# Performance work log

Measured on AMD Instinct MI355X. Metric: run time of the kernel, lower is better.

The kernel has to match this reference:

```python
import jax, jax.numpy as jnp
import numpy as np

NUM_IMU = 72
NUM_NOISE = 12
MAX_PROP = 300
LN_EPS = 1e-5

def _softplus(x):
    return jax.nn.softplus(x)

def setup_inputs() -> dict:
    key = jax.random.key(0)
    k1, k2, k3, k4, k5 = jax.random.split(key, 5)
    d_model = 1024
    seq_len = 4096
    hidden_states = jax.random.normal(k1, (1, seq_len, d_model), dtype=jnp.float32)
    ln_gamma = jnp.ones((d_model,), dtype=jnp.float32)
    ln_beta = jnp.zeros((d_model,), dtype=jnp.float32)
    # Linear: d_model -> NUM_IMU * NUM_NOISE
    W = jax.random.normal(k2, (d_model, NUM_IMU * NUM_NOISE), dtype=jnp.float32) / np.sqrt(d_model)
    b = jax.random.normal(k3, (NUM_IMU * NUM_NOISE,), dtype=jnp.float32) * 0.01
    return {"hidden_states": hidden_states, "ln_gamma": ln_gamma, "ln_beta": ln_beta, "W": W, "b": b}

def _forward(hidden_states, ln_gamma, ln_beta, W, b):
    seq_len = hidden_states.shape[1]
    tsteps = min(MAX_PROP, seq_len)
    x = hidden_states[0]  # [seq, d_model] (squeeze batch=1)
    mu = jnp.mean(x, axis=-1, keepdims=True)
    var = jnp.mean((x - mu) ** 2, axis=-1, keepdims=True)
    xn = (x - mu) * jax.lax.rsqrt(var + LN_EPS) * ln_gamma + ln_beta
    # noise params: [seq, NUM_NOISE, NUM_IMU]
    p = (xn @ W + b).reshape(seq_len, NUM_NOISE, NUM_IMU)
    c = p[:, 4, :]
    c_theta = p[:, 5, :]
    phi = p[:, 6, :]
    phi_theta = p[:, 7, :]
    d = _softplus(p[:, 1, :])
    k = d ** 2 / 4 + _softplus(p[:, 0, :])
    d_theta = _softplus(p[:, 3, :])
    k_theta = d_theta ** 2 / 4 + _softplus(p[:, 2, :])
    acc_base = p[:, 8, :].T      # [imu, seq]
    acc_std = _softplus(p[:, 9, :]).T
    gyro_base = p[:, 10, :].T
    gyro_std = _softplus(p[:, 11, :]).T
    # vectorize over imu: move to [imu, seq, 1]
    def I(a):
        return a.T[:, :, None]
    t = jnp.arange(tsteps, dtype=jnp.float32)[None, None, :]  # [1,1,tstep]
    k_, d_, phi_, c_ = I(k), I(d), I(phi), I(c)
    kt_, dt_, pht_, ct_ = I(k_theta), I(d_theta), I(phi_theta), I(c_theta)
    omega1 = jnp.sqrt(k_ * 4 - d_ ** 2) / 2
    lin = c_ * jnp.exp(-d_ / 2 * t) * jnp.sin(t * omega1 + phi_)
    omega2 = jnp.sqrt(kt_ * 4 - dt_ ** 2) / 2
    ang = ct_ * jnp.exp(-dt_ / 2 * t) * jnp.sin(t * omega2 + pht_)
    spring = lin + ang  # [imu, seq, tstep]
    # banded scatter-add: out[s+t] += spring[:, s, t] for s+t < seq_len
    pos = jnp.arange(seq_len, dtype=jnp.int32)[:, None] + jnp.arange(tsteps, dtype=jnp.int32)[None, :]
    pos_flat = pos.reshape(-1)
    mask = pos_flat < seq_len
    pos_safe = jnp.where(mask, pos_flat, 0)
    vals = spring.reshape(NUM_IMU, -1) * mask.astype(spring.dtype)
    kinematics = jnp.zeros((NUM_IMU, seq_len), dtype=spring.dtype).at[:, pos_safe].add(vals)
    return kinematics, acc_base, acc_std, gyro_base, gyro_std

def reference(hidden_states, ln_gamma, ln_beta, W, b):
    return _forward(hidden_states, ln_gamma, ln_beta, W, b)
```

## Files before the change

### kernel.cpp

```cpp
#include <hip/hip_runtime.h>
#include <hip/hip_bf16.h>
#include <math.h>

#define SEQ 4096
#define DM  1024
#define NIMU 72
#define NNOISE 12
#define NJ (NIMU*NNOISE)
#define TSTEPS 300
#define PLANE (NIMU*SEQ)

#define A2F_SHORTS ((size_t)128 * 128 * 512)
#define BTF_SHORTS ((size_t)28 * 128 * 512)

typedef __attribute__((ext_vector_type(8))) short bf16x8;
typedef __attribute__((ext_vector_type(16))) float f32x16;
typedef __attribute__((ext_vector_type(4))) float f32x4;
typedef __attribute__((ext_vector_type(2))) float f32x2;

__device__ __forceinline__ float softplus_f(float x) {
    return fmaxf(x, 0.f) + log1pf(expf(-fabsf(x)));
}

__device__ __forceinline__ void split_bf16(float x, short& hi, short& lo) {
    unsigned b = __float_as_uint(x);
    unsigned h = (b + 0x7FFFu + ((b >> 16) & 1u)) >> 16;
    float hf = __uint_as_float(h << 16);
    float r = x - hf;
    unsigned b2 = __float_as_uint(r);
    unsigned l2 = (b2 + 0x7FFFu + ((b2 >> 16) & 1u)) >> 16;
    hi = (short)h;
    lo = (short)l2;
}

__global__ __launch_bounds__(512) void ln_kernel(const float* __restrict__ x,
                                                 const float* __restrict__ gamma,
                                                 const float* __restrict__ beta,
                                                 short* __restrict__ A2f) {
    const int tid = threadIdx.x;
    const int row = blockIdx.x * 16 + (tid >> 5);
    const int c   = tid & 31;
    const float4* xr = (const float4*)(x + (size_t)row * DM);

    float s = 0.f, sq = 0.f;
    #pragma unroll
    for (int i = 0; i < 8; ++i) {
        float4 v = xr[c + 32 * i];
        s  += v.x + v.y + v.z + v.w;
        sq += v.x*v.x + v.y*v.y + v.z*v.z + v.w*v.w;
    }
    #pragma unroll
    for (int off = 1; off < 32; off <<= 1) {
        s  += __shfl_xor(s, off);
        sq += __shfl_xor(sq, off);
    }
    const float mean = s * (1.f / DM);
    const float var  = sq * (1.f / DM) - mean * mean;
    const float rstd = rsqrtf(fmaxf(var, 0.f) + 1e-5f);

    const int s_tile = row >> 5, r = row & 31;
    #pragma unroll
    for (int i = 0; i < 8; ++i) {
        const int c4 = c + 32 * i;
        float4 v  = xr[c4];
        float4 gm = ((const float4*)gamma)[c4];
        float4 bt = ((const float4*)beta)[c4];
        float o[4];
        o[0] = (v.x - mean) * rstd * gm.x + bt.x;
        o[1] = (v.y - mean) * rstd * gm.y + bt.y;
        o[2] = (v.z - mean) * rstd * gm.z + bt.z;
        o[3] = (v.w - mean) * rstd * gm.w + bt.w;
        short4 hv, lv;
        split_bf16(o[0], hv.x, lv.x);
        split_bf16(o[1], hv.y, lv.y);
        split_bf16(o[2], hv.z, lv.z);
        split_bf16(o[3], hv.w, lv.w);
        const int ch = c4 >> 2;
        const int g  = (c4 >> 1) & 1;
        const int o4 = (c4 & 1) * 4;
        const size_t base = ((size_t)s_tile * 128 + ch) * 512 + (g * 32 + r) * 8 + o4;
        *(short4*)(A2f + base)                    = hv;
        *(short4*)(A2f + base + (size_t)64 * 512) = lv;
    }
}

__global__ __launch_bounds__(256) void wprep_kernel(const float* __restrict__ W,
                                                    short* __restrict__ Btf) {
    __shared__ float T[32][33];
    const int k0 = blockIdx.x * 32, j0 = blockIdx.y * 32;
    const int t = threadIdx.x;
    {
        const int r = t >> 3, c4 = (t & 7) * 4;
        float4 v = *(const float4*)(W + (size_t)(k0 + r) * NJ + j0 + c4);
        T[r][c4 + 0] = v.x; T[r][c4 + 1] = v.y; T[r][c4 + 2] = v.z; T[r][c4 + 3] = v.w;
    }
    __syncthreads();
    if (t < 128) {
        const int q = t >> 6;
        const int l = t & 63;
        const int n = l & 31, g = l >> 5;
        const int jt = blockIdx.y;
        const int ch = blockIdx.x * 2 + q;
        bf16x8 hv, lv;
        #pragma unroll
        for (int o = 0; o < 8; ++o) {
            short h, lo_;
            split_bf16(T[q * 16 + g * 8 + o][n], h, lo_);
            hv[o] = h; lv[o] = lo_;
        }
        short* dh = Btf + ((size_t)jt * 128 + ch) * 512 + l * 8;
        *(bf16x8*)dh = hv;
        *(bf16x8*)(dh + (size_t)64 * 512) = lv;
    }
}

__global__ __launch_bounds__(256, 2) void gemm_kernel(const short* __restrict__ A2f,
                                                      const short* __restrict__ Btf,
                                                      const float* __restrict__ bias,
                                                      float* __restrict__ ptA,
                                                      float* __restrict__ ptB) {
    const int bid = blockIdx.x;
    const int c = bid & 7, u = bid >> 3;
    const int kh = u / 28, v = u - kh * 28;
    const int bxi = v / 7, by = v - bxi * 7;
    const int bx = c * 4 + bxi;
    const int l = threadIdx.x & 63, w = threadIdx.x >> 6;
    const int mt0 = bx * 4 + (w & 1) * 2;
    const int jt0 = by * 4 + (w >> 1) * 2;
    const int ch0 = kh * 32;
    const short* aB = A2f + (size_t)mt0 * (128 * 512) + l * 8;
    const short* bB = Btf + (size_t)jt0 * (128 * 512) + l * 8;

    f32x16 acc[2][2] = {};
    bf16x8 ah[2][2], al[2][2], bh[2][2], bl[2][2];

    auto ldstep = [&](int slot, int i) {
        const size_t chh = ch0 + i, chl = chh + 64;
        #pragma unroll
        for (int t = 0; t < 2; ++t) {
            ah[slot][t] = *(const bf16x8*)(aB + ((size_t)t * 128 + chh) * 512);
            al[slot][t] = *(const bf16x8*)(aB + ((size_t)t * 128 + chl) * 512);
            bh[slot][t] = *(const bf16x8*)(bB + ((size_t)t * 128 + chh) * 512);
            bl[slot][t] = *(const bf16x8*)(bB + ((size_t)t * 128 + chl) * 512);
        }
    };

    ldstep(0, 0);
    #pragma unroll 2
    for (int i = 0; i < 32; ++i) {
        const int cur = i & 1;
        if (i + 1 < 32) ldstep(cur ^ 1, i + 1);
        #pragma unroll
        for (int mi = 0; mi < 2; ++mi)
            #pragma unroll
            for (int ni = 0; ni < 2; ++ni)
                acc[mi][ni] = __builtin_amdgcn_mfma_f32_32x32x16_bf16(
                    ah[cur][mi], bh[cur][ni], acc[mi][ni], 0, 0, 0);
        #pragma unroll
        for (int mi = 0; mi < 2; ++mi)
            #pragma unroll
            for (int ni = 0; ni < 2; ++ni)
                acc[mi][ni] = __builtin_amdgcn_mfma_f32_32x32x16_bf16(
                    ah[cur][mi], bl[cur][ni], acc[mi][ni], 0, 0, 0);
        #pragma unroll
        for (int mi = 0; mi < 2; ++mi)
            #pragma unroll
            for (int ni = 0; ni < 2; ++ni)
                acc[mi][ni] = __builtin_amdgcn_mfma_f32_32x32x16_bf16(
                    al[cur][mi], bh[cur][ni], acc[mi][ni], 0, 0, 0);
    }

    float* ptH = kh ? ptB : ptA;
    const int jn = l & 31, hi5 = l >> 5;
    #pragma unroll
    for (int ni = 0; ni < 2; ++ni) {
        const int jt = jt0 + ni;
        if (jt < 27) {
            const int j = jt * 32 + jn;
            const float bj = (kh == 0) ? bias[j] : 0.f;
            #pragma unroll
            for (int mi = 0; mi < 2; ++mi) {
                #pragma unroll
                for (int q = 0; q < 4; ++q) {
                    f32x4 o;
                    o[0] = acc[mi][ni][q * 4 + 0] + bj;
                    o[1] = acc[mi][ni][q * 4 + 1] + bj;
                    o[2] = acc[mi][ni][q * 4 + 2] + bj;
                    o[3] = acc[mi][ni][q * 4 + 3] + bj;
                    const int s = (mt0 + mi) * 32 + q * 8 + hi5 * 4;
                    *(f32x4*)(ptH + (size_t)j * SEQ + s) = o;
                }
            }
        }
    }
}

__global__ __launch_bounds__(256) void spring_kernel(const float* __restrict__ ptA,
                                                     const float* __restrict__ ptB,
                                                     float* __restrict__ kin) {
    __shared__ float w3[3][4 * 368];
    const int tid  = threadIdx.x;
    const int lane = tid & 63;
    const int wid  = tid >> 6;
    const int s0   = blockIdx.x * 256;
    const int imu  = blockIdx.y;
    const int s    = s0 + (wid << 6) + lane;

    #pragma unroll
    for (int b = 0; b < 3; ++b)
        #pragma unroll
        for (int i = 0; i < 6; ++i) {
            const int idx = lane + i * 64;
            if (idx < 363) w3[b][wid * 368 + idx] = 0.f;
        }

    const int base = imu * SEQ + s;
    const float p0  = ptA[(size_t)0 * PLANE + base] + ptB[(size_t)0 * PLANE + base];
    const float p1  = ptA[(size_t)1 * PLANE + base] + ptB[(size_t)1 * PLANE + base];
    const float p2  = ptA[(size_t)2 * PLANE + base] + ptB[(size_t)2 * PLANE + base];
    const float p3  = ptA[(size_t)3 * PLANE + base] + ptB[(size_t)3 * PLANE + base];
    const float c1  = ptA[(size_t)4 * PLANE + base] + ptB[(size_t)4 * PLANE + base];
    const float c2  = ptA[(size_t)5 * PLANE + base] + ptB[(size_t)5 * PLANE + base];
    const float ph1 = ptA[(size_t)6 * PLANE + base] + ptB[(size_t)6 * PLANE + base];
    const float ph2 = ptA[(size_t)7 * PLANE + base] + ptB[(size_t)7 * PLANE + base];

    float dd = softplus_f(p1);
    float kk = dd * dd * 0.25f + softplus_f(p0);
    float om1 = 0.5f * sqrtf(fmaxf(4.f * kk - dd * dd, 0.f));
    float dt = softplus_f(p3);
    float kt = dt * dt * 0.25f + softplus_f(p2);
    float om2 = 0.5f * sqrtf(fmaxf(4.f * kt - dt * dt, 0.f));
    float e1 = expf(-0.5f * dd), e2 = expf(-0.5f * dt);
    float sn, cs, sn2, cs2;
    sincosf(om1, &sn, &cs);
    sincosf(om2, &sn2, &cs2);
    f32x2 Rr = {e1 * cs, e2 * cs2};
    f32x2 Ri = {e1 * sn, e2 * sn2};
    sincosf(ph1, &sn, &cs);
    sincosf(ph2, &sn2, &cs2);
    f32x2 zr = {c1 * cs, c2 * cs2};
    f32x2 zi = {c1 * sn, c2 * sn2};

    f32x2 zrB, ziB;
    {
        f32x2 prr = Rr, pri = Ri;
        f32x2 qr = {1.f, 1.f}, qi = {0.f, 0.f};
        int e = 150;
        while (e) {
            if (e & 1) {
                f32x2 nr = qr * prr - qi * pri;
                qi = qr * pri + qi * prr;
                qr = nr;
            }
            f32x2 nr = prr * prr - pri * pri;
            pri = 2.f * prr * pri;
            prr = nr;
            e >>= 1;
        }
        f32x2 nr = zr * qr - zi * qi;
        ziB = zr * qi + zi * qr;
        zrB = nr;
    }

    float* q0 = &w3[0][wid * 368 + lane];
    float* q1 = &w3[1][wid * 368 + lane];
    float* q2 = &w3[2][wid * 368 + lane];

    #pragma unroll 1
    for (int j = 0; j < 150; j += 3) {
        float vA0 = zi.x + zi.y;
        { f32x2 nr = zr * Rr - zi * Ri; zi = zr * Ri + zi * Rr; zr = nr; }
        float vA1 = zi.x + zi.y;
        { f32x2 nr = zr * Rr - zi * Ri; zi = zr * Ri + zi * Rr; zr = nr; }
        float vA2 = zi.x + zi.y;
        { f32x2 nr = zr * Rr - zi * Ri; zi = zr * Ri + zi * Rr; zr = nr; }
        float vB0 = ziB.x + ziB.y;
        { f32x2 nr = zrB * Rr - ziB * Ri; ziB = zrB * Ri + ziB * Rr; zrB = nr; }
        float vB1 = ziB.x + ziB.y;
        { f32x2 nr = zrB * Rr - ziB * Ri; ziB = zrB * Ri + ziB * Rr; zrB = nr; }
        float vB2 = ziB.x + ziB.y;
        { f32x2 nr = zrB * Rr - ziB * Ri; ziB = zrB * Ri + ziB * Rr; zrB = nr; }

        const float a0 = q0[j],     b0 = q0[j + 150];
        const float a1 = q1[j + 1], b1 = q1[j + 151];
        const float a2 = q2[j + 2], b2 = q2[j + 152];
        q0[j]       = a0 + vA0;  q0[j + 150] = b0 + vB0;
        q1[j + 1]   = a1 + vA1;  q1[j + 151] = b1 + vB1;
        q2[j + 2]   = a2 + vA2;  q2[j + 152] = b2 + vB2;
        __asm__ volatile("" ::: "memory");
    }

    __syncthreads();
    for (int i = tid; i < 555; i += 256) {
        float sum = 0.f;
        #pragma unroll
        for (int w = 0; w < 4; ++w) {
            const int idx = i - (w << 6);
            if (idx >= 0 && idx < 363) {
                const int o = w * 368 + idx;
                sum += w3[0][o] + w3[1][o] + w3[2][o];
            }
        }
        const int pos = s0 + i;
        if (pos < SEQ) {
            (void)__hip_atomic_fetch_add(&kin[(size_t)imu * SEQ + pos], sum,
                                         __ATOMIC_RELAXED, __HIP_MEMORY_SCOPE_AGENT);
        }
    }
}

__global__ __launch_bounds__(256) void tail_kernel(const float* __restrict__ ptA,
                                                   const float* __restrict__ ptB,
                                                   float* __restrict__ out) {
    const int i4 = blockIdx.x * 256 + threadIdx.x;
    if (i4 >= PLANE) return;
    const float4 a = ((const float4*)(ptA + (size_t)8 * PLANE))[i4];
    const float4 b = ((const float4*)(ptB + (size_t)8 * PLANE))[i4];
    float4 v;
    v.x = a.x + b.x; v.y = a.y + b.y; v.z = a.z + b.z; v.w = a.w + b.w;
    const int q = (int)(((size_t)i4 * 4) / PLANE);
    if (q & 1) {
        v.x = softplus_f(v.x); v.y = softplus_f(v.y);
        v.z = softplus_f(v.z); v.w = softplus_f(v.w);
    }
    ((float4*)(out + (size_t)PLANE))[i4] = v;
}

extern "C" void kernel_launch(void* const* d_in, const int* in_sizes, int n_in,
                              void* d_out, int out_size, void* d_ws, size_t ws_size,
                              hipStream_t stream) {
    const float* hs    = (const float*)d_in[0];
    const float* gamma = (const float*)d_in[1];
    const float* beta  = (const float*)d_in[2];
    const float* W     = (const float*)d_in[3];
    const float* b     = (const float*)d_in[4];
    float* out = (float*)d_out;

    short* A2f = (short*)d_ws;
    short* Btf = A2f + A2F_SHORTS;
    float* ptA = (float*)(Btf + BTF_SHORTS);
    float* ptB = ptA + (size_t)12 * PLANE;

    hipMemsetAsync(out, 0, (size_t)PLANE * sizeof(float), stream);

    ln_kernel<<<SEQ / 16, 512, 0, stream>>>(hs, gamma, beta, A2f);
    wprep_kernel<<<dim3(DM / 32, NJ / 32), 256, 0, stream>>>(W, Btf);
    gemm_kernel<<<448, 256, 0, stream>>>(A2f, Btf, b, ptA, ptB);
    spring_kernel<<<dim3(SEQ / 256, NIMU), 256, 0, stream>>>(ptA, ptB, out);
    tail_kernel<<<(PLANE + 255) / 256, 256, 0, stream>>>(ptA, ptB, out);
}
```

Measured before the change: 144.0 us.

## Stage GEMM tiles through LDS with direct global-to-LDS loads

Replaces per-wave direct global loads of A/B fragments with block-cooperative staging into a double-buffered LDS tile using global_load_lds. Each tile is then read from LDS by the waves that share it. This removes the redundant global/L2 traffic that came from each wave reloading the same fragments. It adds __syncthreads per iteration and LDS usage, which could reduce overlap or occupancy.

```diff
diff --git a/kernel.cpp b/kernel.cpp
--- a/kernel.cpp
+++ b/kernel.cpp
@@ -31,6 +31,13 @@
     unsigned l2 = (b2 + 0x7FFFu + ((b2 >> 16) & 1u)) >> 16;
     hi = (short)h;
     lo = (short)l2;
+}
+
+__device__ __forceinline__ void gload_lds16(const void* g, void* l) {
+    __builtin_amdgcn_global_load_lds(
+        (const __attribute__((address_space(1))) unsigned int*)g,
+        (__attribute__((address_space(3))) unsigned int*)l,
+        16, 0, 0);
 }
 
 __global__ __launch_bounds__(512) void ln_kernel(const float* __restrict__ x,
@@ -119,55 +126,69 @@
                                                       const float* __restrict__ bias,
                                                       float* __restrict__ ptA,
                                                       float* __restrict__ ptB) {
+    __shared__ bf16x8 lds[2][32][64];
+
     const int bid = blockIdx.x;
     const int c = bid & 7, u = bid >> 3;
     const int kh = u / 28, v = u - kh * 28;
     const int bxi = v / 7, by = v - bxi * 7;
     const int bx = c * 4 + bxi;
     const int l = threadIdx.x & 63, w = threadIdx.x >> 6;
-    const int mt0 = bx * 4 + (w & 1) * 2;
-    const int jt0 = by * 4 + (w >> 1) * 2;
+    const int bx4 = bx * 4, by4 = by * 4;
+    const int mt0 = bx4 + (w & 1) * 2;
+    const int jt0 = by4 + (w >> 1) * 2;
     const int ch0 = kh * 32;
-    const short* aB = A2f + (size_t)mt0 * (128 * 512) + l * 8;
-    const short* bB = Btf + (size_t)jt0 * (128 * 512) + l * 8;
+
+    const int schl = w >> 1;
+    const bool sA  = (w & 1) == 0;
+
+    auto stage = [&](int buf, int it) {
+        const int ch = ch0 + it * 2 + schl;
+        #pragma unroll
+        for (int i = 0; i < 8; ++i) {
+            const int tt = i >> 1, part = i & 1;
+            const short* src = sA
+                ? A2f + ((size_t)(bx4 + tt) * 128 + ch + part * 64) * 512 + l * 8
+                : Btf + ((size_t)(by4 + tt) * 128 + ch + part * 64) * 512 + l * 8;
+            gload_lds16(src, &lds[buf][schl * 16 + (sA ? 0 : 8) + i][0]);
+        }
+    };
 
     f32x16 acc[2][2] = {};
-    bf16x8 ah[2][2], al[2][2], bh[2][2], bl[2][2];
-
-    auto ldstep = [&](int slot, int i) {
-        const size_t chh = ch0 + i, chl = chh + 64;
-        #pragma unroll
-        for (int t = 0; t < 2; ++t) {
-            ah[slot][t] = *(const bf16x8*)(aB + ((size_t)t * 128 + chh) * 512);
-            al[slot][t] = *(const bf16x8*)(aB + ((size_t)t * 128 + chl) * 512);
-            bh[slot][t] = *(const bf16x8*)(bB + ((size_t)t * 128 + chh) * 512);
-            bl[slot][t] = *(const bf16x8*)(bB + ((size_t)t * 128 + chl) * 512);
-        }
-    };
-
-    ldstep(0, 0);
-    #pragma unroll 2
-    for (int i = 0; i < 32; ++i) {
-        const int cur = i & 1;
-        if (i + 1 < 32) ldstep(cur ^ 1, i + 1);
-        #pragma unroll
-        for (int mi = 0; mi < 2; ++mi)
-            #pragma unroll
-            for (int ni = 0; ni < 2; ++ni)
-                acc[mi][ni] = __builtin_amdgcn_mfma_f32_32x32x16_bf16(
-                    ah[cur][mi], bh[cur][ni], acc[mi][ni], 0, 0, 0);
-        #pragma unroll
-        for (int mi = 0; mi < 2; ++mi)
-            #pragma unroll
-            for (int ni = 0; ni < 2; ++ni)
-                acc[mi][ni] = __builtin_amdgcn_mfma_f32_32x32x16_bf16(
-                    ah[cur][mi], bl[cur][ni], acc[mi][ni], 0, 0, 0);
-        #pragma unroll
-        for (int mi = 0; mi < 2; ++mi)
-            #pragma unroll
-            for (int ni = 0; ni < 2; ++ni)
-                acc[mi][ni] = __builtin_amdgcn_mfma_f32_32x32x16_bf16(
-                    al[cur][mi], bh[cur][ni], acc[mi][ni], 0, 0, 0);
+    const int wa = (w & 1) * 2;
+    const int wb = (w >> 1) * 2;
+
+    stage(0, 0);
+    __syncthreads();
+
+    for (int it = 0; it < 16; ++it) {
+        const int cur = it & 1;
+        if (it + 1 < 16) stage(cur ^ 1, it + 1);
+        #pragma unroll
+        for (int chl = 0; chl < 2; ++chl) {
+            const int gb = chl * 16;
+            bf16x8 a0h = lds[cur][gb + (wa + 0) * 2 + 0][l];
+            bf16x8 a0l = lds[cur][gb + (wa + 0) * 2 + 1][l];
+            bf16x8 a1h = lds[cur][gb + (wa + 1) * 2 + 0][l];
+            bf16x8 a1l = lds[cur][gb + (wa + 1) * 2 + 1][l];
+            bf16x8 b0h = lds[cur][gb + 8 + (wb + 0) * 2 + 0][l];
+            bf16x8 b0l = lds[cur][gb + 8 + (wb + 0) * 2 + 1][l];
+            bf16x8 b1h = lds[cur][gb + 8 + (wb + 1) * 2 + 0][l];
+            bf16x8 b1l = lds[cur][gb + 8 + (wb + 1) * 2 + 1][l];
+            acc[0][0] = __builtin_amdgcn_mfma_f32_32x32x16_bf16(a0h, b0h, acc[0][0], 0, 0, 0);
+            acc[0][1] = __builtin_amdgcn_mfma_f32_32x32x16_bf16(a0h, b1h, acc[0][1], 0, 0, 0);
+            acc[1][0] = __builtin_amdgcn_mfma_f32_32x32x16_bf16(a1h, b0h, acc[1][0], 0, 0, 0);
+            acc[1][1] = __builtin_amdgcn_mfma_f32_32x32x16_bf16(a1h, b1h, acc[1][1], 0, 0, 0);
+            acc[0][0] = __builtin_amdgcn_mfma_f32_32x32x16_bf16(a0h, b0l, acc[0][0], 0, 0, 0);
+            acc[0][1] = __builtin_amdgcn_mfma_f32_32x32x16_bf16(a0h, b1l, acc[0][1], 0, 0, 0);
+            acc[1][0] = __builtin_amdgcn_mfma_f32_32x32x16_bf16(a1h, b0l, acc[1][0], 0, 0, 0);
+            acc[1][1] = __builtin_amdgcn_mfma_f32_32x32x16_bf16(a1h, b1l, acc[1][1], 0, 0, 0);
+            acc[0][0] = __builtin_amdgcn_mfma_f32_32x32x16_bf16(a0l, b0h, acc[0][0], 0, 0, 0);
+            acc[0][1] = __builtin_amdgcn_mfma_f32_32x32x16_bf16(a0l, b1h, acc[0][1], 0, 0, 0);
+            acc[1][0] = __builtin_amdgcn_mfma_f32_32x32x16_bf16(a1l, b0h, acc[1][0], 0, 0, 0);
+            acc[1][1] = __builtin_amdgcn_mfma_f32_32x32x16_bf16(a1l, b1h, acc[1][1], 0, 0, 0);
+        }
+        __syncthreads();
     }
 
     float* ptH = kh ? ptB : ptA;
```

Measured after the change: 138.7 us. 3.7% less time.
